# Performance work log

Hardware: AMD Instinct MI355X
Metric: run time of the kernel (lower is better)

## Reference

```python
import jax, jax.numpy as jnp
import numpy as np

DIM = 512

def setup_inputs() -> dict:
    key = jax.random.key(0)
    ks = jax.random.split(key, 6)
    B, S, D = 4, 4096, DIM
    x = jax.random.normal(ks[0], (B, S, D), dtype=jnp.float32)
    mask = jax.random.randint(ks[1], (B, 1, S), 0, 2, dtype=jnp.int32)
    Wqkv = jax.random.normal(ks[2], (D, 3 * D), dtype=jnp.float32) * (1.0 / np.sqrt(D))
    bqkv = jax.random.normal(ks[3], (3 * D,), dtype=jnp.float32) * 0.01
    Wo = jax.random.normal(ks[4], (D, D), dtype=jnp.float32) * (1.0 / np.sqrt(D))
    bo = jax.random.normal(ks[5], (D,), dtype=jnp.float32) * 0.01
    return {"x": x, "mask": mask, "Wqkv": Wqkv, "bqkv": bqkv, "Wo": Wo, "bo": bo}

def reference(x, mask, Wqkv, bqkv, Wo, bo):
    # x: [B, S, D]; mask: [B, 1, S] (broadcast over query dim)
    qkv = x @ Wqkv + bqkv                      # [B, S, 3D]
    q, k, v = jnp.split(qkv, 3, axis=-1)       # each [B, S, D]
    scale = 1.0 / jnp.sqrt(jnp.asarray(DIM, dtype=x.dtype))
    score = jnp.einsum('bqd,bkd->bqk', q, k) * scale   # [B, S, S]
    score = jnp.where(mask == 0, jnp.asarray(-1000.0, dtype=x.dtype), score)
    attn = jax.nn.softmax(score, axis=-1)
    out = jnp.einsum('bqk,bkd->bqd', attn, v)  # [B, S, D]
    return out @ Wo + bo
```

## Files before the change

### kernel.cpp

```cpp
#include <hip/hip_runtime.h>


typedef short bf16x8 __attribute__((ext_vector_type(8)));
typedef float f32x4  __attribute__((ext_vector_type(4)));

#define LOG2E      1.4426950408889634f
#define QKV_SCALE  0.04419417382415922f

typedef __attribute__((address_space(1))) const unsigned int gas_u32;
typedef __attribute__((address_space(3))) unsigned int las_u32;

__device__ __forceinline__ void gload16(const void* g, void* l) {
  __builtin_amdgcn_global_load_lds(
      (gas_u32*)g, (las_u32*)(unsigned int)(uintptr_t)l, 16, 0, 0);
}

__device__ __forceinline__ unsigned short f2bf(float f) {
  unsigned int u = __builtin_bit_cast(unsigned int, f);
  u += 0x7fffu + ((u >> 16) & 1u);
  return (unsigned short)(u >> 16);
}
__device__ __forceinline__ float bf2f(unsigned int u16) {
  unsigned int x = u16 << 16;
  return __builtin_bit_cast(float, x);
}


__global__ __launch_bounds__(256) void cast_x_k(
    const float* __restrict__ x, unsigned short* __restrict__ xb, int n4) {
  int i = blockIdx.x * 256 + threadIdx.x;
  if (i >= n4) return;
  float4 f = ((const float4*)x)[i];
  ushort4 o;
  o.x = f2bf(f.x); o.y = f2bf(f.y); o.z = f2bf(f.z); o.w = f2bf(f.w);
  ((ushort4*)xb)[i] = o;
}

__global__ __launch_bounds__(256) void transpose_cast_k(
    const float* __restrict__ in, unsigned short* __restrict__ outp, int N) {
  __shared__ float tile[32][33];
  const int n0 = blockIdx.x * 32;
  const int k0 = blockIdx.y * 32;
  const int tx = threadIdx.x, ty = threadIdx.y;
  #pragma unroll
  for (int r = 0; r < 32; r += 8)
    tile[ty + r][tx] = in[(size_t)(k0 + ty + r) * N + n0 + tx];
  __syncthreads();
  #pragma unroll
  for (int r = 0; r < 32; r += 8)
    outp[(size_t)(n0 + ty + r) * 512 + k0 + tx] = f2bf(tile[tx][ty + r]);
}


template <int MODE>
__global__ __launch_bounds__(256, 4) void gemm_k(
    const unsigned short* __restrict__ A,
    const unsigned short* __restrict__ Bt,
    void* __restrict__ C,
    unsigned short* __restrict__ out2,
    unsigned short* __restrict__ out3,
    const float* __restrict__ bias,
    const int* __restrict__ mask,
    int M, int N, int K,
    long long sA, long long sB, long long sC) {
  const int bz = blockIdx.z;
  A  += (size_t)bz * sA;
  Bt += (size_t)bz * sB;
  const int bm = blockIdx.x, bn = blockIdx.y;
  const int tid = threadIdx.x;
  const int w = tid >> 6, lane = tid & 63;
  const int g = lane >> 4, li = lane & 15;
  const int wm = w >> 1, wn = w & 1;

  __shared__ __align__(16) unsigned short At[128 * 32];
  __shared__ __align__(16) unsigned short Bs[128 * 32];

  f32x4 acc[4][4] = {};

  const int u0 = tid, u1 = tid + 256;
  const unsigned short* gA0 = A  + (size_t)(bm * 128 + (u0 >> 2)) * K + (u0 & 3) * 8;
  const unsigned short* gA1 = A  + (size_t)(bm * 128 + (u1 >> 2)) * K + (u1 & 3) * 8;
  const unsigned short* gB0 = Bt + (size_t)(bn * 128 + (u0 >> 2)) * K + (u0 & 3) * 8;
  const unsigned short* gB1 = Bt + (size_t)(bn * 128 + (u1 >> 2)) * K + (u1 & 3) * 8;
  unsigned short* lA0 = &At[u0 * 8];
  unsigned short* lA1 = &At[u1 * 8];
  unsigned short* lB0 = &Bs[u0 * 8];
  unsigned short* lB1 = &Bs[u1 * 8];

  for (int k0 = 0; k0 < K; k0 += 32) {
    __syncthreads();
    gload16(gA0, lA0);
    gload16(gA1, lA1);
    gload16(gB0, lB0);
    gload16(gB1, lB1);
    gA0 += 32; gA1 += 32; gB0 += 32; gB1 += 32;
    __syncthreads();
    bf16x8 af[4], bfr[4];
    #pragma unroll
    for (int mf = 0; mf < 4; ++mf)
      af[mf] = *(const bf16x8*)&At[(wm * 64 + mf * 16 + li) * 32 + g * 8];
    #pragma unroll
    for (int nf = 0; nf < 4; ++nf)
      bfr[nf] = *(const bf16x8*)&Bs[(wn * 64 + nf * 16 + li) * 32 + g * 8];
    #pragma unroll
    for (int mf = 0; mf < 4; ++mf)
      #pragma unroll
      for (int nf = 0; nf < 4; ++nf)
        acc[mf][nf] = __builtin_amdgcn_mfma_f32_16x16x32_bf16(
            af[mf], bfr[nf], acc[mf][nf], 0, 0, 0);
  }

  const int colbase = bn * 128 + wn * 64;
  const int rowbase = bm * 128 + wm * 64;

  if constexpr (MODE == 0) {
    unsigned short* qb = (unsigned short*)C;
    #pragma unroll
    for (int nf = 0; nf < 4; ++nf) {
      const int col = colbase + nf * 16 + li;
      const float bv = bias[col];
      #pragma unroll
      for (int mf = 0; mf < 4; ++mf) {
        const int row0 = rowbase + mf * 16 + g * 4;
        if (col < 512) {
          #pragma unroll
          for (int r = 0; r < 4; ++r)
            qb[(size_t)(row0 + r) * 512 + col] =
                f2bf((acc[mf][nf][r] + bv) * QKV_SCALE);
        } else if (col < 1024) {
          #pragma unroll
          for (int r = 0; r < 4; ++r)
            out2[(size_t)(row0 + r) * 512 + (col - 512)] =
                f2bf(acc[mf][nf][r] + bv);
        } else {
          const int bb = row0 >> 12, s = row0 & 4095;
          ushort4 v;
          v.x = f2bf(acc[mf][nf][0] + bv);
          v.y = f2bf(acc[mf][nf][1] + bv);
          v.z = f2bf(acc[mf][nf][2] + bv);
          v.w = f2bf(acc[mf][nf][3] + bv);
          *(ushort4*)&out3[(size_t)(bb * 512 + (col - 1024)) * 4096 + s] = v;
        }
      }
    }
  } else if constexpr (MODE == 1) {
    unsigned short* Cs = (unsigned short*)C + (size_t)bz * sC;
    #pragma unroll
    for (int nf = 0; nf < 4; ++nf) {
      const int col = colbase + nf * 16 + li;
      const int mv = mask[bz * N + col];
      #pragma unroll
      for (int mf = 0; mf < 4; ++mf) {
        const int row0 = rowbase + mf * 16 + g * 4;
        #pragma unroll
        for (int r = 0; r < 4; ++r) {
          float v = (mv == 0) ? -1000.0f : acc[mf][nf][r];
          Cs[(size_t)(row0 + r) * N + col] = f2bf(v);
        }
      }
    }
  } else if constexpr (MODE == 2) {
    unsigned short* Cs = (unsigned short*)C + (size_t)bz * sC;
    #pragma unroll
    for (int nf = 0; nf < 4; ++nf) {
      const int col = colbase + nf * 16 + li;
      #pragma unroll
      for (int mf = 0; mf < 4; ++mf) {
        const int row0 = rowbase + mf * 16 + g * 4;
        #pragma unroll
        for (int r = 0; r < 4; ++r)
          Cs[(size_t)(row0 + r) * N + col] = f2bf(acc[mf][nf][r]);
      }
    }
  } else {
    float* Cf = (float*)C;
    #pragma unroll
    for (int nf = 0; nf < 4; ++nf) {
      const int col = colbase + nf * 16 + li;
      const float bv = bias[col];
      #pragma unroll
      for (int mf = 0; mf < 4; ++mf) {
        const int row0 = rowbase + mf * 16 + g * 4;
        #pragma unroll
        for (int r = 0; r < 4; ++r)
          Cf[(size_t)(row0 + r) * N + col] = acc[mf][nf][r] + bv;
      }
    }
  }
}

__global__ __launch_bounds__(256) void softmax_k(unsigned short* __restrict__ SP) {
  const size_t base = (size_t)blockIdx.x * 4096;
  const int tid = threadIdx.x;
  __shared__ float red[8];

  const unsigned short* p = SP + base + tid * 16;
  uint4 a = *(const uint4*)p;
  uint4 b = *(const uint4*)(p + 8);
  unsigned int u[8] = {a.x, a.y, a.z, a.w, b.x, b.y, b.z, b.w};
  float v[16];
  #pragma unroll
  for (int i = 0; i < 8; ++i) {
    v[2 * i]     = bf2f(u[i] & 0xffffu);
    v[2 * i + 1] = bf2f(u[i] >> 16);
  }
  float m = v[0];
  #pragma unroll
  for (int i = 1; i < 16; ++i) m = fmaxf(m, v[i]);
  #pragma unroll
  for (int off = 1; off < 64; off <<= 1) m = fmaxf(m, __shfl_xor(m, off));
  if ((tid & 63) == 0) red[tid >> 6] = m;
  __syncthreads();
  m = fmaxf(fmaxf(red[0], red[1]), fmaxf(red[2], red[3]));

  float s = 0.f;
  float pv[16];
  #pragma unroll
  for (int i = 0; i < 16; ++i) {
    pv[i] = exp2f((v[i] - m) * LOG2E);
    s += pv[i];
  }
  #pragma unroll
  for (int off = 1; off < 64; off <<= 1) s += __shfl_xor(s, off);
  if ((tid & 63) == 0) red[4 + (tid >> 6)] = s;
  __syncthreads();
  s = red[4] + red[5] + red[6] + red[7];
  const float inv = 1.0f / s;

  #pragma unroll
  for (int i = 0; i < 8; ++i)
    u[i] = (unsigned int)f2bf(pv[2 * i] * inv) |
           ((unsigned int)f2bf(pv[2 * i + 1] * inv) << 16);
  unsigned short* q = SP + base + tid * 16;
  *(uint4*)q = make_uint4(u[0], u[1], u[2], u[3]);
  *(uint4*)(q + 8) = make_uint4(u[4], u[5], u[6], u[7]);
}


extern "C" void kernel_launch(void* const* d_in, const int* in_sizes, int n_in,
                              void* d_out, int out_size, void* d_ws, size_t ws_size,
                              hipStream_t stream) {
  const float* x    = (const float*)d_in[0];
  const int*   mask = (const int*)d_in[1];
  const float* Wqkv = (const float*)d_in[2];
  const float* bqkv = (const float*)d_in[3];
  const float* Wo   = (const float*)d_in[4];
  const float* bo   = (const float*)d_in[5];
  float* out = (float*)d_out;

  const size_t SZ_TOK = 16777216;
  char* ws = (char*)d_ws;
  unsigned short* xb  = (unsigned short*)(ws + 0 * SZ_TOK);
  unsigned short* qb  = (unsigned short*)(ws + 1 * SZ_TOK);
  unsigned short* kb  = (unsigned short*)(ws + 2 * SZ_TOK);
  unsigned short* vT  = (unsigned short*)(ws + 3 * SZ_TOK);
  unsigned short* ao  = (unsigned short*)(ws + 4 * SZ_TOK);
  unsigned short* Wtq = (unsigned short*)(ws + 5 * SZ_TOK);
  unsigned short* Wto = (unsigned short*)(ws + 5 * SZ_TOK + 1572864);
  unsigned short* Sb  = (unsigned short*)(ws + 5 * SZ_TOK + 2097152);
  if (ws_size < (size_t)220200960) return;

  cast_x_k<<<8192, 256, 0, stream>>>(x, xb, 2097152);
  transpose_cast_k<<<dim3(48, 16), dim3(32, 8), 0, stream>>>(Wqkv, Wtq, 1536);
  transpose_cast_k<<<dim3(16, 16), dim3(32, 8), 0, stream>>>(Wo, Wto, 512);

  gemm_k<0><<<dim3(128, 12, 1), 256, 0, stream>>>(
      xb, Wtq, (void*)qb, kb, vT, bqkv, (const int*)nullptr,
      16384, 1536, 512, 0LL, 0LL, 0LL);

  gemm_k<1><<<dim3(32, 32, 4), 256, 0, stream>>>(
      qb, kb, (void*)Sb, nullptr, nullptr, nullptr, mask,
      4096, 4096, 512, 2097152LL, 2097152LL, 16777216LL);

  softmax_k<<<16384, 256, 0, stream>>>(Sb);

  gemm_k<2><<<dim3(32, 4, 4), 256, 0, stream>>>(
      Sb, vT, (void*)ao, nullptr, nullptr, nullptr, nullptr,
      4096, 512, 4096, 16777216LL, 2097152LL, 2097152LL);

  gemm_k<3><<<dim3(128, 4, 1), 256, 0, stream>>>(
      ao, Wto, (void*)out, nullptr, nullptr, bo, nullptr,
      16384, 512, 512, 0LL, 0LL, 0LL);
}
```

Before: 390.7 us.

## Fuse softmax exp into QK GEMM epilogue, defer normalization, double-buffer LDS

The QK^T GEMM epilogue now writes exp(score) directly, with no max subtraction and masked entries set to 0. It also emits per-tile partial row sums into a workspace buffer. A tiny rowsum kernel turns these into reciprocals, and the PV GEMM scales its output by them. This removes the separate softmax pass, which read and wrote the full 4096x4096 bf16 score matrix per batch. The GEMM main loop is also double-buffered so the next K-slice loads while MFMAs run. The risk is overflow, since exp runs without the max shift and relies on scores staying small for these inputs. The larger LDS footprint may also lower occupancy.

```diff
diff --git a/kernel.cpp b/kernel.cpp
--- a/kernel.cpp
+++ b/kernel.cpp
@@ -61,6 +61,7 @@
     unsigned short* __restrict__ out3,
     const float* __restrict__ bias,
     const int* __restrict__ mask,
+    float* __restrict__ aux,
     int M, int N, int K,
     long long sA, long long sB, long long sC) {
   const int bz = blockIdx.z;
@@ -72,8 +73,8 @@
   const int g = lane >> 4, li = lane & 15;
   const int wm = w >> 1, wn = w & 1;
 
-  __shared__ __align__(16) unsigned short At[128 * 32];
-  __shared__ __align__(16) unsigned short Bs[128 * 32];
+  __shared__ __align__(16) unsigned short At[2][128 * 32];
+  __shared__ __align__(16) unsigned short Bs[2][128 * 32];
 
   f32x4 acc[4][4] = {};
 
@@ -82,32 +83,40 @@
   const unsigned short* gA1 = A  + (size_t)(bm * 128 + (u1 >> 2)) * K + (u1 & 3) * 8;
   const unsigned short* gB0 = Bt + (size_t)(bn * 128 + (u0 >> 2)) * K + (u0 & 3) * 8;
   const unsigned short* gB1 = Bt + (size_t)(bn * 128 + (u1 >> 2)) * K + (u1 & 3) * 8;
-  unsigned short* lA0 = &At[u0 * 8];
-  unsigned short* lA1 = &At[u1 * 8];
-  unsigned short* lB0 = &Bs[u0 * 8];
-  unsigned short* lB1 = &Bs[u1 * 8];
-
-  for (int k0 = 0; k0 < K; k0 += 32) {
-    __syncthreads();
-    gload16(gA0, lA0);
-    gload16(gA1, lA1);
-    gload16(gB0, lB0);
-    gload16(gB1, lB1);
-    gA0 += 32; gA1 += 32; gB0 += 32; gB1 += 32;
-    __syncthreads();
+
+  const int NT = K >> 5;
+
+  gload16(gA0, &At[0][u0 * 8]);
+  gload16(gA1, &At[0][u1 * 8]);
+  gload16(gB0, &Bs[0][u0 * 8]);
+  gload16(gB1, &Bs[0][u1 * 8]);
+  gA0 += 32; gA1 += 32; gB0 += 32; gB1 += 32;
+  __syncthreads();
+
+  for (int t = 0; t < NT; ++t) {
+    const int cur = t & 1;
+    if (t + 1 < NT) {
+      const int nxt = cur ^ 1;
+      gload16(gA0, &At[nxt][u0 * 8]);
+      gload16(gA1, &At[nxt][u1 * 8]);
+      gload16(gB0, &Bs[nxt][u0 * 8]);
+      gload16(gB1, &Bs[nxt][u1 * 8]);
+      gA0 += 32; gA1 += 32; gB0 += 32; gB1 += 32;
+    }
     bf16x8 af[4], bfr[4];
     #pragma unroll
     for (int mf = 0; mf < 4; ++mf)
-      af[mf] = *(const bf16x8*)&At[(wm * 64 + mf * 16 + li) * 32 + g * 8];
+      af[mf] = *(const bf16x8*)&At[cur][(wm * 64 + mf * 16 + li) * 32 + g * 8];
     #pragma unroll
     for (int nf = 0; nf < 4; ++nf)
-      bfr[nf] = *(const bf16x8*)&Bs[(wn * 64 + nf * 16 + li) * 32 + g * 8];
+      bfr[nf] = *(const bf16x8*)&Bs[cur][(wn * 64 + nf * 16 + li) * 32 + g * 8];
     #pragma unroll
     for (int mf = 0; mf < 4; ++mf)
       #pragma unroll
       for (int nf = 0; nf < 4; ++nf)
         acc[mf][nf] = __builtin_amdgcn_mfma_f32_16x16x32_bf16(
             af[mf], bfr[nf], acc[mf][nf], 0, 0, 0);
+    if (t + 1 < NT) __syncthreads();
   }
 
   const int colbase = bn * 128 + wn * 64;
@@ -145,6 +154,7 @@
     }
   } else if constexpr (MODE == 1) {
     unsigned short* Cs = (unsigned short*)C + (size_t)bz * sC;
+    float rsum[4][4] = {};
     #pragma unroll
     for (int nf = 0; nf < 4; ++nf) {
       const int col = colbase + nf * 16 + li;
@@ -154,13 +164,34 @@
         const int row0 = rowbase + mf * 16 + g * 4;
         #pragma unroll
         for (int r = 0; r < 4; ++r) {
-          float v = (mv == 0) ? -1000.0f : acc[mf][nf][r];
-          Cs[(size_t)(row0 + r) * N + col] = f2bf(v);
+          float p = (mv == 0) ? 0.0f : exp2f(acc[mf][nf][r] * LOG2E);
+          const unsigned short pb = f2bf(p);
+          Cs[(size_t)(row0 + r) * N + col] = pb;
+          rsum[mf][r] += bf2f((unsigned int)pb);
         }
       }
     }
+    #pragma unroll
+    for (int mf = 0; mf < 4; ++mf)
+      #pragma unroll
+      for (int r = 0; r < 4; ++r) {
+        float s = rsum[mf][r];
+        s += __shfl_xor(s, 1);
+        s += __shfl_xor(s, 2);
+        s += __shfl_xor(s, 4);
+        s += __shfl_xor(s, 8);
+        if (li == 0)
+          aux[((size_t)bz * 4096 + rowbase + mf * 16 + g * 4 + r) * 64 +
+              bn * 2 + wn] = s;
+      }
   } else if constexpr (MODE == 2) {
     unsigned short* Cs = (unsigned short*)C + (size_t)bz * sC;
+    float iv[4][4];
+    #pragma unroll
+    for (int mf = 0; mf < 4; ++mf)
+      #pragma unroll
+      for (int r = 0; r < 4; ++r)
+        iv[mf][r] = bias[(size_t)bz * 4096 + rowbase + mf * 16 + g * 4 + r];
     #pragma unroll
     for (int nf = 0; nf < 4; ++nf) {
       const int col = colbase + nf * 16 + li;
@@ -169,7 +200,7 @@
         const int row0 = rowbase + mf * 16 + g * 4;
         #pragma unroll
         for (int r = 0; r < 4; ++r)
-          Cs[(size_t)(row0 + r) * N + col] = f2bf(acc[mf][nf][r]);
+          Cs[(size_t)(row0 + r) * N + col] = f2bf(acc[mf][nf][r] * iv[mf][r]);
       }
     }
   } else {
@@ -189,51 +220,17 @@
   }
 }
 
-__global__ __launch_bounds__(256) void softmax_k(unsigned short* __restrict__ SP) {
-  const size_t base = (size_t)blockIdx.x * 4096;
-  const int tid = threadIdx.x;
-  __shared__ float red[8];
-
-  const unsigned short* p = SP + base + tid * 16;
-  uint4 a = *(const uint4*)p;
-  uint4 b = *(const uint4*)(p + 8);
-  unsigned int u[8] = {a.x, a.y, a.z, a.w, b.x, b.y, b.z, b.w};
-  float v[16];
-  #pragma unroll
-  for (int i = 0; i < 8; ++i) {
-    v[2 * i]     = bf2f(u[i] & 0xffffu);
-    v[2 * i + 1] = bf2f(u[i] >> 16);
-  }
-  float m = v[0];
-  #pragma unroll
-  for (int i = 1; i < 16; ++i) m = fmaxf(m, v[i]);
-  #pragma unroll
-  for (int off = 1; off < 64; off <<= 1) m = fmaxf(m, __shfl_xor(m, off));
-  if ((tid & 63) == 0) red[tid >> 6] = m;
-  __syncthreads();
-  m = fmaxf(fmaxf(red[0], red[1]), fmaxf(red[2], red[3]));
-
+__global__ __launch_bounds__(256) void rowsum_k(
+    const float* __restrict__ partial, float* __restrict__ inv) {
+  const int row = blockIdx.x * 256 + threadIdx.x;
+  const float4* p = (const float4*)(partial + (size_t)row * 64);
   float s = 0.f;
-  float pv[16];
   #pragma unroll
   for (int i = 0; i < 16; ++i) {
-    pv[i] = exp2f((v[i] - m) * LOG2E);
-    s += pv[i];
+    float4 v = p[i];
+    s += (v.x + v.y) + (v.z + v.w);
   }
-  #pragma unroll
-  for (int off = 1; off < 64; off <<= 1) s += __shfl_xor(s, off);
-  if ((tid & 63) == 0) red[4 + (tid >> 6)] = s;
-  __syncthreads();
-  s = red[4] + red[5] + red[6] + red[7];
-  const float inv = 1.0f / s;
-
-  #pragma unroll
-  for (int i = 0; i < 8; ++i)
-    u[i] = (unsigned int)f2bf(pv[2 * i] * inv) |
-           ((unsigned int)f2bf(pv[2 * i + 1] * inv) << 16);
-  unsigned short* q = SP + base + tid * 16;
-  *(uint4*)q = make_uint4(u[0], u[1], u[2], u[3]);
-  *(uint4*)(q + 8) = make_uint4(u[4], u[5], u[6], u[7]);
+  inv[row] = 1.0f / s;
 }
 
 
@@ -258,6 +255,8 @@
   unsigned short* Wtq = (unsigned short*)(ws + 5 * SZ_TOK);
   unsigned short* Wto = (unsigned short*)(ws + 5 * SZ_TOK + 1572864);
   unsigned short* Sb  = (unsigned short*)(ws + 5 * SZ_TOK + 2097152);
+  float* partial = (float*)(ws + 0);
+  float* inv     = (float*)(ws + 4194304);
   if (ws_size < (size_t)220200960) return;
 
   cast_x_k<<<8192, 256, 0, stream>>>(x, xb, 2097152);
@@ -265,20 +264,20 @@
   transpose_cast_k<<<dim3(16, 16), dim3(32, 8), 0, stream>>>(Wo, Wto, 512);
 
   gemm_k<0><<<dim3(128, 12, 1), 256, 0, stream>>>(
-      xb, Wtq, (void*)qb, kb, vT, bqkv, (const int*)nullptr,
+      xb, Wtq, (void*)qb, kb, vT, bqkv, (const int*)nullptr, nullptr,
       16384, 1536, 512, 0LL, 0LL, 0LL);
 
   gemm_k<1><<<dim3(32, 32, 4), 256, 0, stream>>>(
-      qb, kb, (void*)Sb, nullptr, nullptr, nullptr, mask,
+      qb, kb, (void*)Sb, nullptr, nullptr, nullptr, mask, partial,
       4096, 4096, 512, 2097152LL, 2097152LL, 16777216LL);
 
-  softmax_k<<<16384, 256, 0, stream>>>(Sb);
+  rowsum_k<<<64, 256, 0, stream>>>(partial, inv);
 
   gemm_k<2><<<dim3(32, 4, 4), 256, 0, stream>>>(
-      Sb, vT, (void*)ao, nullptr, nullptr, nullptr, nullptr,
+      Sb, vT, (void*)ao, nullptr, nullptr, inv, nullptr, nullptr,
       4096, 512, 4096, 16777216LL, 2097152LL, 2097152LL);
 
   gemm_k<3><<<dim3(128, 4, 1), 256, 0, stream>>>(
-      ao, Wto, (void*)out, nullptr, nullptr, bo, nullptr,
+      ao, Wto, (void*)out, nullptr, nullptr, bo, nullptr, nullptr,
       16384, 512, 512, 0LL, 0LL, 0LL);
 }
```

New measurement: 359.6 us. 8.0% less time.
